# Optimization experiments

Measured on AMD Instinct MI355X. Metric: run time of the kernel, lower is better.

## Reference

```python
import jax, jax.numpy as jnp
import numpy as np

OUT, IN, GS = 11008, 4096, 128   # out_features, in_features, group_size
G = IN // GS                     # num_groups = 32 (in_features divisible by group_size)
TOKENS = 8192                    # batch 4 * seq 2048


def setup_inputs() -> dict:
    key = jax.random.key(0)
    k1, k2, k3, k4, k5 = jax.random.split(key, 5)
    x = jax.random.normal(k1, (TOKENS, IN), dtype=jnp.float32)
    # packed int4 weights: two nibbles per byte, stored as int32 in [0,256)
    qweight = jax.random.randint(k2, (OUT, IN // 2), 0, 256, dtype=jnp.int32)
    # realistic GPTQ scales (small positive) and zero-points in [0,15]
    scales = jax.random.uniform(k3, (OUT, G), dtype=jnp.float32) * 0.01 + 1e-3
    zeros = jax.random.uniform(k4, (OUT, G), dtype=jnp.float32) * 15.0
    bias = jax.random.normal(k5, (OUT,), dtype=jnp.float32) * 0.01
    return {"x": x, "qweight": qweight, "scales": scales, "zeros": zeros, "bias": bias}


def _dequant(qweight, scales, zeros):
    # unpack: column 2i = low nibble, column 2i+1 = high nibble (matches torch loop)
    low = (qweight & 15).astype(jnp.float32)          # [OUT, IN/2]
    high = ((qweight >> 4) & 15).astype(jnp.float32)  # [OUT, IN/2]
    w = jnp.stack([low, high], axis=-1).reshape(OUT, IN)
    # group-wise dequant: (q - zero) * scale per group of GS input channels
    w = (w.reshape(OUT, G, GS) - zeros[:, :, None]) * scales[:, :, None]
    return w.reshape(OUT, IN)


def reference(x, qweight, scales, zeros, bias):
    w = _dequant(qweight, scales, zeros)   # [OUT, IN] fp32
    # F.linear: x @ w.T + bias
    return jnp.einsum('ti,oi->to', x, w) + bias
```

## Files before the change

### kernel.cpp

```cpp
#include <hip/hip_runtime.h>
#include <stdint.h>

#define OUTF 11008
#define INF  4096
#define NG   32
#define TOK  8192
#define KB4  2048

#define BM 128
#define BN 256
#define BK 64
#define NT (INF / BK)
#define GX (OUTF / BN)
#define GY (TOK / BM)
#define NWG (GX * GY)

typedef unsigned short u16;
typedef __attribute__((ext_vector_type(8))) short bf16x8;
typedef __attribute__((ext_vector_type(4))) float f32x4;
typedef __attribute__((ext_vector_type(16))) float f32x16;
typedef __attribute__((ext_vector_type(4))) int i32x4;

__device__ inline u16 f2bf(float f) {
  union { float f; uint32_t u; } v; v.f = f;
  return (u16)((v.u + 0x7fff + ((v.u >> 16) & 1)) >> 16);
}

__device__ inline void async_copy16(const void* g, const void* l) {
  __builtin_amdgcn_global_load_lds(
      (__attribute__((address_space(1))) void*)(g),
      (__attribute__((address_space(3))) void*)(l), 16, 0, 0);
}

#define FENCE() asm volatile("" ::: "memory")
#define BAR()   do { FENCE(); __builtin_amdgcn_s_barrier(); FENCE(); } while (0)
#define VMCNT(n) asm volatile("s_waitcnt vmcnt(" #n ")" ::: "memory")


#define NXU ((long long)TOK * INF / 4)
#define NWU ((long long)OUTF * KB4 / 4)
#define PREPBLK 2048

__global__ __launch_bounds__(256) void prep(const float* __restrict__ X,
                                            const int* __restrict__ QW,
                                            const float* __restrict__ scales,
                                            const float* __restrict__ zeros,
                                            u16* __restrict__ Xb,
                                            u16* __restrict__ Wb) {
  const long long stride = (long long)gridDim.x * 256;
  for (long long i = (long long)blockIdx.x * 256 + threadIdx.x; i < NXU + NWU;
       i += stride) {
    if (i < NXU) {
      const f32x4 f = __builtin_nontemporal_load((const f32x4*)X + i);
      union { u16 t[4]; uint2 v; } u;
      u.t[0] = f2bf(f[0]); u.t[1] = f2bf(f[1]);
      u.t[2] = f2bf(f[2]); u.t[3] = f2bf(f[3]);
      ((uint2*)Xb)[i] = u.v;
    } else {
      const long long j = i - NXU;
      const int o = (int)(j >> 9);
      const int c0 = ((int)j & 511) * 4;
      const int g = c0 >> 6;
      const float s = scales[o * NG + g];
      const float zs = -zeros[o * NG + g] * s;
      const i32x4 q = __builtin_nontemporal_load((const i32x4*)QW + j);
      union { u16 t[8]; int4 v; } u;
#pragma unroll
      for (int k = 0; k < 4; ++k) {
        u.t[2 * k]     = f2bf(fmaf((float)(q[k] & 15), s, zs));
        u.t[2 * k + 1] = f2bf(fmaf((float)((q[k] >> 4) & 15), s, zs));
      }
      ((int4*)Wb)[j] = u.v;
    }
  }
}


__global__ __launch_bounds__(512, 4) void gemm_occ2(const u16* __restrict__ A,
                                                    const u16* __restrict__ B,
                                                    const float* __restrict__ bias,
                                                    float* __restrict__ C) {
  __shared__ __align__(16) u16 As[BM * BK];
  __shared__ __align__(16) u16 Bs[2][BN * BK];
  const int tid = threadIdx.x;
  const int lane = tid & 63;
  const int wid = __builtin_amdgcn_readfirstlane(tid >> 6);

  const int lin = blockIdx.x;
  const int xcd = lin & 7;
  const int wgc = lin >> 3;
  int bmr, bn;
  if (wgc < 320) {
    const int g = wgc >> 6, r = wgc & 63;
    bn = g * 8 + (r & 7);
    bmr = r >> 3;
  } else {
    const int r = wgc - 320;
    bn = 40 + r % 3;
    bmr = r / 3;
  }
  const int bm = xcd * 8 + bmr;

  const u16* Ab = A + (size_t)bm * BM * INF;
  const u16* Bb = B + (size_t)bn * BN * INF;

  const int rowoff = tid >> 3;
  const int gran = (tid & 7) ^ (rowoff & 7) ^ ((rowoff >> 3) & 3);
  const u16* Asrc = Ab + (size_t)rowoff * INF + gran * 8;
  const u16* Bsrc = Bb + (size_t)rowoff * INF + gran * 8;
  const int wid8 = wid * 8;

  const int rr32 = lane & 31;
  const int hi = lane >> 5;
  const int xr = (rr32 & 7) ^ ((rr32 >> 3) & 3);
  const int wm = wid >> 2;
  const int wn = wid & 3;

  f32x16 acc[2][2] = {};

#define STAGE1(LDS, SRC, TT, R0)                                               \
  async_copy16((SRC) + (size_t)(R0) * INF + (size_t)(TT) * BK,                 \
               (const char*)(LDS) + ((R0) + wid8) * 128);

#define RD_A2(DST, KG)                                                         \
  _Pragma("unroll") for (int mt = 0; mt < 2; ++mt)                             \
    DST[mt] = *(const bf16x8*)&As[(wm * 64 + mt * 32 + rr32) * BK +            \
                                  ((((KG) * 2 + hi) ^ xr) * 8)];
#define RD_B2(DST, S, KG)                                                      \
  _Pragma("unroll") for (int nt = 0; nt < 2; ++nt)                             \
    DST[nt] = *(const bf16x8*)&Bs[S][(wn * 64 + nt * 32 + rr32) * BK +         \
                                     ((((KG) * 2 + hi) ^ xr) * 8)];

#define KGPHASE(S, KG)                                                         \
  do {                                                                         \
    bf16x8 af[2], bf[2];                                                       \
    RD_A2(af, KG) RD_B2(bf, S, KG)                                             \
    __builtin_amdgcn_s_setprio(1);                                             \
    _Pragma("unroll") for (int mt = 0; mt < 2; ++mt)                           \
      _Pragma("unroll") for (int nt = 0; nt < 2; ++nt)                         \
        acc[mt][nt] = __builtin_amdgcn_mfma_f32_32x32x16_bf16(                 \
            af[mt], bf[nt], acc[mt][nt], 0, 0, 0);                             \
    __builtin_amdgcn_s_setprio(0);                                             \
  } while (0)

  STAGE1(&As[0], Asrc, 0, 0)      STAGE1(&As[0], Asrc, 0, 64)
  STAGE1(&Bs[0][0], Bsrc, 0, 0)   STAGE1(&Bs[0][0], Bsrc, 0, 64)
  STAGE1(&Bs[0][0], Bsrc, 0, 128) STAGE1(&Bs[0][0], Bsrc, 0, 192)
  STAGE1(&Bs[1][0], Bsrc, 1, 0)   STAGE1(&Bs[1][0], Bsrc, 1, 64)
  STAGE1(&Bs[1][0], Bsrc, 1, 128) STAGE1(&Bs[1][0], Bsrc, 1, 192)
  VMCNT(4);
  BAR();

  for (int t = 0; t < NT; ++t) {
    const int S = t & 1;
    KGPHASE(S, 0); KGPHASE(S, 1); KGPHASE(S, 2); KGPHASE(S, 3);
    BAR();
    if (t + 1 < NT) { STAGE1(&As[0], Asrc, t + 1, 0) STAGE1(&As[0], Asrc, t + 1, 64) }
    if (t + 2 < NT) {
      STAGE1(&Bs[S][0], Bsrc, t + 2, 0)   STAGE1(&Bs[S][0], Bsrc, t + 2, 64)
      STAGE1(&Bs[S][0], Bsrc, t + 2, 128) STAGE1(&Bs[S][0], Bsrc, t + 2, 192)
      VMCNT(4);
    } else {
      VMCNT(0);
    }
    BAR();
  }

  float bv[2];
#pragma unroll
  for (int nt = 0; nt < 2; ++nt)
    bv[nt] = bias[bn * BN + wn * 64 + nt * 32 + rr32];
#pragma unroll
  for (int mt = 0; mt < 2; ++mt)
#pragma unroll
    for (int nt = 0; nt < 2; ++nt) {
      const int gn = bn * BN + wn * 64 + nt * 32 + rr32;
#pragma unroll
      for (int reg = 0; reg < 16; ++reg) {
        const int gm = bm * BM + wm * 64 + mt * 32 +
                       (reg & 3) + 8 * (reg >> 2) + 4 * hi;
        __builtin_nontemporal_store(acc[mt][nt][reg] + bv[nt],
                                    &C[(size_t)gm * OUTF + gn]);
      }
    }
}


#define FBM 128
#define FBN 128
#define FBK 64

#define FMFMA_COMPUTE()                                                       \
  do {                                                                        \
    const int frr = lane & 15;                                                \
    const int fq4 = lane >> 4;                                                \
    _Pragma("unroll") for (int ks = 0; ks < 2; ++ks) {                        \
      bf16x8 fa[4], fb[4];                                                    \
      const int kk = (((ks * 4 + fq4) ^ (frr & 7)) * 8);                      \
      _Pragma("unroll") for (int i = 0; i < 4; ++i) {                         \
        fa[i] = *(const bf16x8*)&Asf[(mwave + i * 16 + frr) * FBK + kk];      \
        fb[i] = *(const bf16x8*)&Bsf[(nwave + i * 16 + frr) * FBK + kk];      \
      }                                                                       \
      _Pragma("unroll") for (int mi = 0; mi < 4; ++mi)                        \
        _Pragma("unroll") for (int ni = 0; ni < 4; ++ni)                      \
          facc[mi][ni] = __builtin_amdgcn_mfma_f32_16x16x32_bf16(             \
              fa[mi], fb[ni], facc[mi][ni], 0, 0, 0);                         \
    }                                                                         \
  } while (0)

__global__ __launch_bounds__(256) void gemm_fused(const float* __restrict__ X,
                                                  const int* __restrict__ QW,
                                                  const float* __restrict__ scales,
                                                  const float* __restrict__ zeros,
                                                  const float* __restrict__ bias,
                                                  float* __restrict__ C) {
  __shared__ __align__(16) u16 Asf[FBM * FBK];
  __shared__ __align__(16) u16 Bsf[FBN * FBK];
  const int tid = threadIdx.x;
  const int lane = tid & 63;
  const int wid = tid >> 6;
  const int bm = blockIdx.y, bn = blockIdx.x;
  const int row = tid >> 1;
  const int half = tid & 1;
  const float* xr = X + (size_t)(bm * FBM + row) * INF + half * 32;
  const int* qr = QW + (size_t)(bn * FBN + row) * KB4 + half * 16;
  const float* srow = scales + (size_t)(bn * FBN + row) * NG;
  const float* zrow = zeros + (size_t)(bn * FBN + row) * NG;
  const int mwave = (wid >> 1) * 64;
  const int nwave = (wid & 1) * 64;
  f32x4 facc[4][4] = {};

  for (int kb = 0; kb < INF / FBK; ++kb) {
    const int k0 = kb * FBK;
    union { u16 t[32]; int4 v[4]; } ta, tb;
#pragma unroll
    for (int j = 0; j < 8; ++j) {
      const float4 f = *(const float4*)(xr + k0 + j * 4);
      ta.t[4 * j]     = f2bf(f.x);
      ta.t[4 * j + 1] = f2bf(f.y);
      ta.t[4 * j + 2] = f2bf(f.z);
      ta.t[4 * j + 3] = f2bf(f.w);
    }
    {
      const float s = srow[kb >> 1];
      const float zs = -zrow[kb >> 1] * s;
#pragma unroll
      for (int j = 0; j < 4; ++j) {
        const int4 q = *(const int4*)(qr + kb * 32 + j * 4);
        const int qq[4] = {q.x, q.y, q.z, q.w};
#pragma unroll
        for (int u = 0; u < 4; ++u) {
          tb.t[8 * j + 2 * u]     = f2bf(fmaf((float)(qq[u] & 15), s, zs));
          tb.t[8 * j + 2 * u + 1] = f2bf(fmaf((float)((qq[u] >> 4) & 15), s, zs));
        }
      }
    }
    __syncthreads();
#pragma unroll
    for (int j = 0; j < 4; ++j) {
      *(int4*)&Asf[row * FBK + (((half * 4 + j) ^ (row & 7)) * 8)] = ta.v[j];
      *(int4*)&Bsf[row * FBK + (((half * 4 + j) ^ (row & 7)) * 8)] = tb.v[j];
    }
    __syncthreads();
    FMFMA_COMPUTE();
  }
  {
    const int ncol = lane & 15;
    const int qrow = (lane >> 4) * 4;
#pragma unroll
    for (int mi = 0; mi < 4; ++mi)
#pragma unroll
      for (int ni = 0; ni < 4; ++ni) {
        const int gn = bn * FBN + nwave + ni * 16 + ncol;
        const float bvv = bias[gn];
#pragma unroll
        for (int r = 0; r < 4; ++r) {
          const int gm = bm * FBM + mwave + mi * 16 + qrow + r;
          C[(size_t)gm * OUTF + gn] = facc[mi][ni][r] + bvv;
        }
      }
  }
}


extern "C" void kernel_launch(void* const* d_in, const int* in_sizes, int n_in,
                              void* d_out, int out_size, void* d_ws, size_t ws_size,
                              hipStream_t stream) {
  const float* x = (const float*)d_in[0];
  const int* qw = (const int*)d_in[1];
  const float* scales = (const float*)d_in[2];
  const float* zeros = (const float*)d_in[3];
  const float* bias = (const float*)d_in[4];
  float* out = (float*)d_out;

  const size_t needW = (size_t)OUTF * INF * sizeof(u16);
  const size_t needX = (size_t)TOK * INF * sizeof(u16);

  if (ws_size >= needW + needX) {
    u16* Wb = (u16*)d_ws;
    u16* Xb = (u16*)((char*)d_ws + needW);
    prep<<<PREPBLK, 256, 0, stream>>>(x, qw, scales, zeros, Xb, Wb);
    gemm_occ2<<<dim3(NWG), 512, 0, stream>>>(Xb, Wb, bias, out);
  } else {
    gemm_fused<<<dim3(OUTF / FBN, TOK / FBM), 256, 0, stream>>>(x, qw, scales, zeros, bias, out);
  }
}
```

Baseline: 1.125 ms.

## Enlarge M tile to 256 and stream B fragments directly into registers

Doubles the M tile to 256 rows so each workgroup computes a 256x256 output tile with 4x2 MFMA accumulators per wave. B operands are no longer staged through LDS; each wave loads its own B fragments from global memory straight into registers, prefetching the next k-step after each phase. A is double-buffered in LDS instead. This is meant to raise arithmetic intensity and cut LDS traffic for B, at the cost of higher register pressure, occupancy lowered to 2 blocks, and uncoalesced direct global B loads.

```diff
diff --git a/kernel.cpp b/kernel.cpp
--- a/kernel.cpp
+++ b/kernel.cpp
@@ -7,7 +7,7 @@
 #define TOK  8192
 #define KB4  2048
 
-#define BM 128
+#define BM 256
 #define BN 256
 #define BK 64
 #define NT (INF / BK)
@@ -76,12 +76,11 @@
 }
 
 
-__global__ __launch_bounds__(512, 4) void gemm_occ2(const u16* __restrict__ A,
-                                                    const u16* __restrict__ B,
-                                                    const float* __restrict__ bias,
-                                                    float* __restrict__ C) {
-  __shared__ __align__(16) u16 As[BM * BK];
-  __shared__ __align__(16) u16 Bs[2][BN * BK];
+__global__ __launch_bounds__(512, 2) void gemm_bd(const u16* __restrict__ A,
+                                                  const u16* __restrict__ B,
+                                                  const float* __restrict__ bias,
+                                                  float* __restrict__ C) {
+  __shared__ __align__(16) u16 As[2][BM * BK];
   const int tid = threadIdx.x;
   const int lane = tid & 63;
   const int wid = __builtin_amdgcn_readfirstlane(tid >> 6);
@@ -90,24 +89,22 @@
   const int xcd = lin & 7;
   const int wgc = lin >> 3;
   int bmr, bn;
-  if (wgc < 320) {
-    const int g = wgc >> 6, r = wgc & 63;
+  if (wgc < 160) {
+    const int g = wgc >> 5, r = wgc & 31;
     bn = g * 8 + (r & 7);
     bmr = r >> 3;
   } else {
-    const int r = wgc - 320;
+    const int r = wgc - 160;
     bn = 40 + r % 3;
     bmr = r / 3;
   }
-  const int bm = xcd * 8 + bmr;
+  const int bm = xcd * 4 + bmr;
 
   const u16* Ab = A + (size_t)bm * BM * INF;
-  const u16* Bb = B + (size_t)bn * BN * INF;
 
   const int rowoff = tid >> 3;
   const int gran = (tid & 7) ^ (rowoff & 7) ^ ((rowoff >> 3) & 3);
   const u16* Asrc = Ab + (size_t)rowoff * INF + gran * 8;
-  const u16* Bsrc = Bb + (size_t)rowoff * INF + gran * 8;
   const int wid8 = wid * 8;
 
   const int rr32 = lane & 31;
@@ -116,50 +113,60 @@
   const int wm = wid >> 2;
   const int wn = wid & 3;
 
-  f32x16 acc[2][2] = {};
-
-#define STAGE1(LDS, SRC, TT, R0)                                               \
-  async_copy16((SRC) + (size_t)(R0) * INF + (size_t)(TT) * BK,                 \
-               (const char*)(LDS) + ((R0) + wid8) * 128);
-
-#define RD_A2(DST, KG)                                                         \
-  _Pragma("unroll") for (int mt = 0; mt < 2; ++mt)                             \
-    DST[mt] = *(const bf16x8*)&As[(wm * 64 + mt * 32 + rr32) * BK +            \
-                                  ((((KG) * 2 + hi) ^ xr) * 8)];
-#define RD_B2(DST, S, KG)                                                      \
-  _Pragma("unroll") for (int nt = 0; nt < 2; ++nt)                             \
-    DST[nt] = *(const bf16x8*)&Bs[S][(wn * 64 + nt * 32 + rr32) * BK +         \
-                                     ((((KG) * 2 + hi) ^ xr) * 8)];
-
-#define KGPHASE(S, KG)                                                         \
+  const u16* Bb0 = B + (size_t)(bn * BN + wn * 64 + rr32) * INF + hi * 8;
+  const u16* Bb1 = Bb0 + (size_t)32 * INF;
+
+  f32x16 acc[4][2] = {};
+  bf16x8 breg[4][2];
+
+#define STAGE_A(S, TT)                                                         \
   do {                                                                         \
-    bf16x8 af[2], bf[2];                                                       \
-    RD_A2(af, KG) RD_B2(bf, S, KG)                                             \
+    async_copy16(Asrc + (size_t)0 * INF + (size_t)(TT) * BK,                   \
+                 (const char*)&As[S][0] + (0 + wid8) * 128);                   \
+    async_copy16(Asrc + (size_t)64 * INF + (size_t)(TT) * BK,                  \
+                 (const char*)&As[S][0] + (64 + wid8) * 128);                  \
+    async_copy16(Asrc + (size_t)128 * INF + (size_t)(TT) * BK,                 \
+                 (const char*)&As[S][0] + (128 + wid8) * 128);                 \
+    async_copy16(Asrc + (size_t)192 * INF + (size_t)(TT) * BK,                 \
+                 (const char*)&As[S][0] + (192 + wid8) * 128);                 \
+  } while (0)
+
+#define LOAD_B(KG, TT)                                                         \
+  do {                                                                         \
+    breg[KG][0] = *(const bf16x8*)(Bb0 + (size_t)(TT) * BK + (KG) * 16);       \
+    breg[KG][1] = *(const bf16x8*)(Bb1 + (size_t)(TT) * BK + (KG) * 16);       \
+  } while (0)
+
+#define PH(S, T, KG)                                                           \
+  do {                                                                         \
+    bf16x8 af[4];                                                              \
+    _Pragma("unroll") for (int mt = 0; mt < 4; ++mt)                           \
+      af[mt] = *(const bf16x8*)&As[S][(wm * 128 + mt * 32 + rr32) * BK +       \
+                                      ((((KG) * 2 + hi) ^ xr) * 8)];           \
     __builtin_amdgcn_s_setprio(1);                                             \
-    _Pragma("unroll") for (int mt = 0; mt < 2; ++mt)                           \
+    _Pragma("unroll") for (int mt = 0; mt < 4; ++mt)                           \
       _Pragma("unroll") for (int nt = 0; nt < 2; ++nt)                         \
         acc[mt][nt] = __builtin_amdgcn_mfma_f32_32x32x16_bf16(                 \
-            af[mt], bf[nt], acc[mt][nt], 0, 0, 0);                             \
+            af[mt], breg[KG][nt], acc[mt][nt], 0, 0, 0);                       \
     __builtin_amdgcn_s_setprio(0);                                             \
+    if ((T) + 1 < NT) { LOAD_B(KG, (T) + 1); }                                 \
   } while (0)
 
-  STAGE1(&As[0], Asrc, 0, 0)      STAGE1(&As[0], Asrc, 0, 64)
-  STAGE1(&Bs[0][0], Bsrc, 0, 0)   STAGE1(&Bs[0][0], Bsrc, 0, 64)
-  STAGE1(&Bs[0][0], Bsrc, 0, 128) STAGE1(&Bs[0][0], Bsrc, 0, 192)
-  STAGE1(&Bs[1][0], Bsrc, 1, 0)   STAGE1(&Bs[1][0], Bsrc, 1, 64)
-  STAGE1(&Bs[1][0], Bsrc, 1, 128) STAGE1(&Bs[1][0], Bsrc, 1, 192)
-  VMCNT(4);
+  STAGE_A(0, 0);
+  STAGE_A(1, 1);
+  LOAD_B(0, 0); LOAD_B(1, 0); LOAD_B(2, 0); LOAD_B(3, 0);
+  VMCNT(12);
   BAR();
 
   for (int t = 0; t < NT; ++t) {
     const int S = t & 1;
-    KGPHASE(S, 0); KGPHASE(S, 1); KGPHASE(S, 2); KGPHASE(S, 3);
+    PH(S, t, 0); PH(S, t, 1); PH(S, t, 2); PH(S, t, 3);
     BAR();
-    if (t + 1 < NT) { STAGE1(&As[0], Asrc, t + 1, 0) STAGE1(&As[0], Asrc, t + 1, 64) }
     if (t + 2 < NT) {
-      STAGE1(&Bs[S][0], Bsrc, t + 2, 0)   STAGE1(&Bs[S][0], Bsrc, t + 2, 64)
-      STAGE1(&Bs[S][0], Bsrc, t + 2, 128) STAGE1(&Bs[S][0], Bsrc, t + 2, 192)
-      VMCNT(4);
+      STAGE_A(S, t + 2);
+      VMCNT(12);
+    } else if (t + 1 < NT) {
+      VMCNT(8);
     } else {
       VMCNT(0);
     }
@@ -171,13 +178,13 @@
   for (int nt = 0; nt < 2; ++nt)
     bv[nt] = bias[bn * BN + wn * 64 + nt * 32 + rr32];
 #pragma unroll
-  for (int mt = 0; mt < 2; ++mt)
+  for (int mt = 0; mt < 4; ++mt)
 #pragma unroll
     for (int nt = 0; nt < 2; ++nt) {
       const int gn = bn * BN + wn * 64 + nt * 32 + rr32;
 #pragma unroll
       for (int reg = 0; reg < 16; ++reg) {
-        const int gm = bm * BM + wm * 64 + mt * 32 +
+        const int gm = bm * BM + wm * 128 + mt * 32 +
                        (reg & 3) + 8 * (reg >> 2) + 4 * hi;
         __builtin_nontemporal_store(acc[mt][nt][reg] + bv[nt],
                                     &C[(size_t)gm * OUTF + gn]);
@@ -300,7 +307,7 @@
     u16* Wb = (u16*)d_ws;
     u16* Xb = (u16*)((char*)d_ws + needW);
     prep<<<PREPBLK, 256, 0, stream>>>(x, qw, scales, zeros, Xb, Wb);
-    gemm_occ2<<<dim3(NWG), 512, 0, stream>>>(Xb, Wb, bias, out);
+    gemm_bd<<<dim3(NWG), 512, 0, stream>>>(Xb, Wb, bias, out);
   } else {
     gemm_fused<<<dim3(OUTF / FBN, TOK / FBM), 256, 0, stream>>>(x, qw, scales, zeros, bias, out);
   }
```

Result: slower. 1.387 ms (+23.3%).
